# Kernel optimization log

Measured on AMD Instinct MI355X. Metric: run time of the kernel, lower is better.

The kernel has to match this reference:

```python
import jax, jax.numpy as jnp
import numpy as np

B = 16384
D = 1024
NG = 64
H = 2  # num_heads = len(conv_kernel_sizes)


def setup_inputs() -> dict:
    key = jax.random.key(0)
    ks = jax.random.split(key, 12)
    s = 0.02
    return {
        "x": jax.random.normal(ks[0], (B, D), jnp.float32),
        "group_labels": jax.random.randint(ks[1], (B,), 0, NG, dtype=jnp.int32),
        "num_groups": NG,
        "conv_w2": jax.random.normal(ks[2], (2,), jnp.float32) * s,
        "conv_b2": jax.random.normal(ks[3], (), jnp.float32) * s,
        "conv_w4": jax.random.normal(ks[4], (4,), jnp.float32) * s,
        "conv_b4": jax.random.normal(ks[5], (), jnp.float32) * s,
        "intra_in_w": jax.random.normal(ks[6], (3 * D, D), jnp.float32) * s,
        "intra_in_b": jnp.zeros((3 * D,), jnp.float32),
        "intra_out_w": jax.random.normal(ks[7], (D, D), jnp.float32) * s,
        "intra_out_b": jnp.zeros((D,), jnp.float32),
        "inter_in_w": jax.random.normal(ks[8], (3 * D, D), jnp.float32) * s,
        "inter_in_b": jnp.zeros((3 * D,), jnp.float32),
        "inter_out_w": jax.random.normal(ks[9], (D, D), jnp.float32) * s,
        "inter_out_b": jnp.zeros((D,), jnp.float32),
        "lin_w": jax.random.normal(ks[10], (D, D), jnp.float32) * s,
        "lin_b": jnp.zeros((D,), jnp.float32),
    }


def _seg_conv(x_s, l_s, w, b):
    """Per-group Conv2d(1,1,(k,1),padding=(k//2,0)) along the group-sorted axis,
    with zero padding at group boundaries and output trimmed to group size.
    out[i] = sum_j w[j] * x[i + j - k//2] if same group else 0."""
    n = x_s.shape[0]
    k = w.shape[0]
    pad = k // 2
    xp = jnp.pad(x_s, ((pad, pad), (0, 0)))
    lp = jnp.pad(l_s, (pad, pad), constant_values=-1)
    out = jnp.zeros_like(x_s)
    for j in range(k):  # k <= 4, static
        m = (lp[j:j + n] == l_s)[:, None]
        out = out + w[j] * jnp.where(m, xp[j:j + n], 0.0)
    return out + b


def _mha_self(xs, in_w, in_b, out_w, out_b, h):
    """torch nn.MultiheadAttention self-attention, seq-first xs: [S, N, D]."""
    S, N, Dm = xs.shape
    dh = Dm // h
    qkv = jnp.einsum('snd,ed->sne', xs, in_w) + in_b
    q, k, v = jnp.split(qkv, 3, axis=-1)
    q = q.reshape(S, N, h, dh)
    k = k.reshape(S, N, h, dh)
    v = v.reshape(S, N, h, dh)
    scores = jnp.einsum('qnhd,knhd->nhqk', q, k) / np.float32(np.sqrt(dh))
    a = jax.nn.softmax(scores, axis=-1)
    o = jnp.einsum('nhqk,knhd->qnhd', a, v).reshape(S, N, Dm)
    return jnp.einsum('snd,ed->sne', o, out_w) + out_b


def reference(x, group_labels, num_groups, conv_w2, conv_b2, conv_w4, conv_b4,
              intra_in_w, intra_in_b, intra_out_w, intra_out_b,
              inter_in_w, inter_in_b, inter_out_w, inter_out_b, lin_w, lin_b):
    n, d = x.shape
    labels = group_labels.astype(jnp.int32)
    perm = jnp.argsort(labels)  # stable: preserves original order within groups
    x_s = x[perm]
    l_s = labels[perm]

    # per-group convs -> [2, N, D] token stack (seq-first for MHA)
    t2 = _seg_conv(x_s, l_s, conv_w2, conv_b2)
    t4 = _seg_conv(x_s, l_s, conv_w4, conv_b4)
    tok = jnp.stack([t2, t4], axis=0)

    # intra attention over the 2 conv tokens per position, mean, then Linear
    intra = _mha_self(tok, intra_in_w, intra_in_b, intra_out_w, intra_out_b, H).mean(axis=0)
    lin_out = intra @ lin_w.T + lin_b  # [N, D]

    # inter-group: seq-len-1 attention over FIRST row of each other group ==
    # out_proj(v_proj(first_row)); mean over the other present groups.
    counts = jax.ops.segment_sum(jnp.ones((n,), jnp.int32), labels, num_segments=num_groups)
    present = counts > 0
    first_idx = jax.ops.segment_min(jnp.arange(n), labels, num_segments=num_groups)
    first_rows = x[jnp.where(present, first_idx, 0)]  # [NG, D]
    Wv = inter_in_w[2 * d:]
    bv = inter_in_b[2 * d:]
    f = (first_rows @ Wv.T + bv) @ inter_out_w.T + inter_out_b  # [NG, D]
    f = jnp.where(present[:, None], f, 0.0)
    n_present = jnp.sum(present.astype(jnp.int32))
    denom = jnp.maximum(n_present - 1, 1).astype(x.dtype)
    inter_mean = (jnp.sum(f, axis=0)[None, :] - f) / denom
    inter_mean = inter_mean * (n_present > 1).astype(x.dtype)

    out_s = lin_out + inter_mean[l_s]
    return jnp.zeros_like(x).at[perm].set(out_s)
```

## Files before the change

kernel.cpp:

```cpp
#include <hip/hip_runtime.h>
#include <hip/hip_bf16.h>

#define B_N 16384
#define D_DIM 1024
#define NGRP 64
#define NCHUNK 64
#define CHUNK 256

typedef __attribute__((ext_vector_type(8))) short short8;
typedef __attribute__((ext_vector_type(8))) unsigned short ushort8;
typedef __attribute__((ext_vector_type(4))) unsigned short ushort4v;
typedef __attribute__((ext_vector_type(4))) float floatx4;

__device__ __forceinline__ float bf2f(unsigned short h) {
    union { unsigned u; float f; } c; c.u = ((unsigned)h) << 16; return c.f;
}
__device__ __forceinline__ unsigned short f2bf(float f) {
    union { float f; unsigned u; } c; c.f = f;
    unsigned r = c.u + 0x7FFFu + ((c.u >> 16) & 1u);
    return (unsigned short)(r >> 16);
}

__device__ __forceinline__ void gload_lds16(const void* g, void* l) {
    __builtin_amdgcn_global_load_lds(
        (const __attribute__((address_space(1))) unsigned int*)g,
        (__attribute__((address_space(3))) unsigned int*)l, 16, 0, 0);
}

__global__ __launch_bounds__(256) void k_hist(const int* __restrict__ labels,
                                              int* __restrict__ hist) {
    __shared__ int lh[NGRP];
    int t = threadIdx.x, c = blockIdx.x;
    if (t < NGRP) lh[t] = 0;
    __syncthreads();
    int lab = labels[c * CHUNK + t];
    atomicAdd(&lh[lab], 1);
    __syncthreads();
    if (t < NGRP) hist[c * NGRP + t] = lh[t];
}

__global__ void k_scan(int* __restrict__ hist, int* __restrict__ gstart,
                       int* __restrict__ counts, float* __restrict__ scal) {
    __shared__ int cnt[NGRP];
    __shared__ int st[NGRP + 1];
    int g = threadIdx.x;
    int run = 0;
    for (int c = 0; c < NCHUNK; c++) {
        int v = hist[c * NGRP + g];
        hist[c * NGRP + g] = run;
        run += v;
    }
    cnt[g] = run;
    counts[g] = run;
    __syncthreads();
    if (g == 0) {
        int s = 0, np = 0;
        for (int i = 0; i < NGRP; i++) { st[i] = s; s += cnt[i]; np += (cnt[i] > 0); }
        st[NGRP] = s;
        scal[0] = (np > 1) ? 1.0f / (float)(np - 1) : 0.0f;
    }
    __syncthreads();
    gstart[g] = st[g];
    if (g == 0) gstart[NGRP] = st[NGRP];
    for (int c = 0; c < NCHUNK; c++) hist[c * NGRP + g] += st[g];
}

__global__ __launch_bounds__(256) void k_scatter(const int* __restrict__ labels,
                                                 const int* __restrict__ hist,
                                                 int* __restrict__ perm,
                                                 int* __restrict__ ls) {
    __shared__ int lab[CHUNK];
    int c = blockIdx.x, t = threadIdx.x;
    int i = c * CHUNK + t;
    int L = labels[i];
    lab[t] = L;
    __syncthreads();
    int rank = 0;
    for (int j = 0; j < t; j++) rank += (lab[j] == L);
    int pos = hist[c * NGRP + L] + rank;
    perm[pos] = i;
    ls[pos] = L;
}

__global__ __launch_bounds__(256) void k_conv(const float* __restrict__ x,
                                              const int* __restrict__ perm,
                                              const int* __restrict__ ls,
                                              const float* __restrict__ w2, const float* __restrict__ b2,
                                              const float* __restrict__ w4, const float* __restrict__ b4,
                                              unsigned short* __restrict__ tok) {
    const int i = blockIdx.x;
    const int li = ls[i];
    const int p0 = perm[i];
    const int pm1 = (i >= 1 && ls[i - 1] == li) ? perm[i - 1] : -1;
    const int pm2 = (i >= 2 && ls[i - 2] == li) ? perm[i - 2] : -1;
    const int pp1 = (i + 1 < B_N && ls[i + 1] == li) ? perm[i + 1] : -1;
    const int c = threadIdx.x * 4;
    floatx4 z = (floatx4)0.0f;
    floatx4 x0 = *(const floatx4*)(x + (size_t)p0 * D_DIM + c);
    floatx4 xm1 = (pm1 >= 0) ? *(const floatx4*)(x + (size_t)pm1 * D_DIM + c) : z;
    floatx4 xm2 = (pm2 >= 0) ? *(const floatx4*)(x + (size_t)pm2 * D_DIM + c) : z;
    floatx4 xp1 = (pp1 >= 0) ? *(const floatx4*)(x + (size_t)pp1 * D_DIM + c) : z;
    const float w20 = w2[0], w21 = w2[1], cb2 = b2[0];
    const float w40 = w4[0], w41 = w4[1], w42 = w4[2], w43 = w4[3], cb4 = b4[0];
    ushort4v o2, o4;
#pragma unroll
    for (int j = 0; j < 4; j++) {
        float t2 = w20 * xm1[j] + w21 * x0[j] + cb2;
        float t4 = w40 * xm2[j] + w41 * xm1[j] + w42 * x0[j] + w43 * xp1[j] + cb4;
        o2[j] = f2bf(t2);
        o4[j] = f2bf(t4);
    }
    *(ushort4v*)(tok + (size_t)(2 * i) * D_DIM + c) = o2;
    *(ushort4v*)(tok + (size_t)(2 * i + 1) * D_DIM + c) = o4;
}

__global__ __launch_bounds__(256) void k_prep(const float* __restrict__ intra_in_w,
                                              const float* __restrict__ lin_w,
                                              const float* __restrict__ intra_out_w,
                                              unsigned short* __restrict__ Wqk,
                                              unsigned short* __restrict__ linwb,
                                              unsigned short* __restrict__ WoT,
                                              unsigned short* __restrict__ WvT) {
    __shared__ float tile[32][33];
    const int bx = blockIdx.x;
    if (bx < 3072) {
        int i = bx * 256 + threadIdx.x;
        const float* src;
        unsigned short* dst;
        int j;
        if (i < 524288) { src = intra_in_w; dst = Wqk; j = i; }
        else { src = lin_w; dst = linwb; j = i - 524288; }
        floatx4 v = *(const floatx4*)(src + (size_t)j * 4);
        ushort4v o;
#pragma unroll
        for (int q = 0; q < 4; q++) o[q] = f2bf(v[q]);
        *(ushort4v*)(dst + (size_t)j * 4) = o;
    } else {
        int tb = bx - 3072;
        const float* src;
        unsigned short* dst;
        if (tb < 1024) { src = intra_out_w; dst = WoT; }
        else { src = intra_in_w + (size_t)2048 * D_DIM; dst = WvT; tb -= 1024; }
        const int bX = (tb & 31) * 32, bY = (tb >> 5) * 32;
        const int tx = threadIdx.x & 31, ty = threadIdx.x >> 5;
        for (int r = ty; r < 32; r += 8)
            tile[r][tx] = src[(size_t)(bY + r) * D_DIM + bX + tx];
        __syncthreads();
        for (int r = ty; r < 32; r += 8)
            dst[(size_t)(bX + r) * D_DIM + bY + tx] = f2bf(tile[tx][r]);
    }
}

__global__ __launch_bounds__(256) void k_ob2(const float* __restrict__ ow,
                                             const float* __restrict__ ob,
                                             const float* __restrict__ bv,
                                             float* __restrict__ ob2) {
    int e = blockIdx.x * 256 + threadIdx.x;
    const floatx4* wr4 = (const floatx4*)(ow + (size_t)e * D_DIM);
    const floatx4* bv4 = (const floatx4*)bv;
    float s = ob[e];
    for (int k4 = 0; k4 < D_DIM / 4; k4++) {
        floatx4 a = wr4[k4], b = bv4[k4];
        s += a[0] * b[0] + a[1] * b[1] + a[2] * b[2] + a[3] * b[3];
    }
    ob2[e] = s;
}

__global__ __launch_bounds__(256) void k_u(const float* __restrict__ x,
                                           const int* __restrict__ perm,
                                           const int* __restrict__ gstart,
                                           const int* __restrict__ counts,
                                           const float* __restrict__ Wfull,
                                           const float* __restrict__ bfull,
                                           float* __restrict__ u,
                                           const float* __restrict__ lin_w,
                                           const float* __restrict__ lin_b,
                                           const float* __restrict__ ob2,
                                           float* __restrict__ biasc) {
    const int g = blockIdx.y;
    const int n = blockIdx.x * 256 + threadIdx.x;
    __shared__ __align__(16) float xr[D_DIM];
    const bool isb = (g == NGRP);
    int row = 0;
    if (!isb) {
        const int cnt = counts[g];
        row = (cnt > 0) ? perm[gstart[g]] : 0;
    }
    for (int k = threadIdx.x; k < D_DIM; k += 256)
        xr[k] = isb ? ob2[k] : x[(size_t)row * D_DIM + k];
    __syncthreads();
    const float* wrow = isb ? (lin_w + (size_t)n * D_DIM)
                            : (Wfull + (size_t)(2 * D_DIM + n) * D_DIM);
    const floatx4* wr4 = (const floatx4*)wrow;
    const floatx4* xr4 = (const floatx4*)xr;
    float s = isb ? lin_b[n] : bfull[2 * D_DIM + n];
    for (int k4 = 0; k4 < D_DIM / 4; k4++) {
        floatx4 a = xr4[k4], b = wr4[k4];
        s += a[0] * b[0] + a[1] * b[1] + a[2] * b[2] + a[3] * b[3];
    }
    if (isb) biasc[n] = s;
    else u[g * D_DIM + n] = s;
}

__global__ __launch_bounds__(256) void k_f(const float* __restrict__ u,
                                           const int* __restrict__ counts,
                                           const float* __restrict__ W,
                                           const float* __restrict__ b,
                                           float* __restrict__ f) {
    const int g = blockIdx.y;
    const int n = blockIdx.x * 256 + threadIdx.x;
    __shared__ __align__(16) float ur[D_DIM];
    const int cnt = counts[g];
    for (int k = threadIdx.x; k < D_DIM; k += 256) ur[k] = u[g * D_DIM + k];
    __syncthreads();
    const floatx4* wr4 = (const floatx4*)(W + (size_t)n * D_DIM);
    const floatx4* ur4 = (const floatx4*)ur;
    float s = b[n];
    for (int k4 = 0; k4 < D_DIM / 4; k4++) {
        floatx4 a = ur4[k4], w = wr4[k4];
        s += a[0] * w[0] + a[1] * w[1] + a[2] * w[2] + a[3] * w[3];
    }
    f[g * D_DIM + n] = (cnt > 0) ? s : 0.0f;
}

__global__ __launch_bounds__(256) void k_imean(const float* __restrict__ f,
                                               const float* __restrict__ scal,
                                               float* __restrict__ im) {
    int c = blockIdx.x * 256 + threadIdx.x;
    float s = 0.0f;
    for (int g = 0; g < NGRP; g++) s += f[g * D_DIM + c];
    float fl = scal[0];
    for (int g = 0; g < NGRP; g++) im[g * D_DIM + c] = (s - f[g * D_DIM + c]) * fl;
}

template <int MODE>
__global__ __launch_bounds__(256)
void gemm_bt(const unsigned short* __restrict__ A,
             const unsigned short* __restrict__ W,
             int M, int N, int K, int lda, int ldw,
             const float* __restrict__ bias,
             unsigned short* __restrict__ outb, int ldc,
             float* __restrict__ outf,
             const int* __restrict__ perm,
             const int* __restrict__ ls,
             const float* __restrict__ imean) {
    __shared__ __align__(16) unsigned short sA[128 * 64];
    __shared__ __align__(16) unsigned short sB[128 * 64];
    const int t = threadIdx.x;
    const int lane = t & 63, wv = t >> 6;
    int bx = blockIdx.x, by = blockIdx.y;
    const int nX = gridDim.x, nY = gridDim.y;
    if ((nY & 7) == 0) {
        const int bid = by * nX + bx;
        const int xcd = bid & 7, j = bid >> 3;
        const int stripe = nY >> 3;
        by = xcd * stripe + j / nX;
        bx = j % nX;
    }
    const int m0 = by * 128, n0 = bx * 128;
    const int wm = (wv & 1) * 64, wn = (wv >> 1) * 64;
    const int l15 = lane & 15, quad = lane >> 4;
    const int sw = l15 & 7;

    floatx4 acc[4][4];
#pragma unroll
    for (int i = 0; i < 4; i++)
#pragma unroll
        for (int j = 0; j < 4; j++) acc[i][j] = (floatx4)0.0f;

    for (int k0 = 0; k0 < K; k0 += 64) {
#pragma unroll
        for (int r = 0; r < 4; r++) {
            const int chunk = r * 256 + wv * 64;
            const int idx = chunk + lane;
            const int row = idx >> 3;
            const int kb = (idx & 7) ^ (row & 7);
            gload_lds16(A + (size_t)(m0 + row) * lda + k0 + kb * 8, &sA[chunk * 8]);
            gload_lds16(W + (size_t)(n0 + row) * ldw + k0 + kb * 8, &sB[chunk * 8]);
        }
        __syncthreads();
#pragma unroll
        for (int kk = 0; kk < 64; kk += 32) {
            const int kc = kk >> 3;
            short8 av[4], bv[4];
#pragma unroll
            for (int mt = 0; mt < 4; mt++)
                av[mt] = *(const short8*)&sA[(wm + mt * 16 + l15) * 64 +
                                             (((kc + quad) ^ sw) << 3)];
#pragma unroll
            for (int nt = 0; nt < 4; nt++)
                bv[nt] = *(const short8*)&sB[(wn + nt * 16 + l15) * 64 +
                                             (((kc + quad) ^ sw) << 3)];
#pragma unroll
            for (int mt = 0; mt < 4; mt++)
#pragma unroll
                for (int nt = 0; nt < 4; nt++)
                    acc[mt][nt] = __builtin_amdgcn_mfma_f32_16x16x32_bf16(
                        av[mt], bv[nt], acc[mt][nt], 0, 0, 0);
        }
        __syncthreads();
    }

    if (MODE == 1) {
#pragma unroll
        for (int nt = 0; nt < 4; nt++) {
            const int gc = n0 + wn + nt * 16 + l15;
#pragma unroll
            for (int mt = 0; mt < 4; mt++) {
                const int gr = m0 + wm + mt * 16 + quad * 4;
#pragma unroll
                for (int r = 0; r < 4; r++)
                    outb[(size_t)(gr + r) * ldc + gc] = f2bf(acc[mt][nt][r]);
            }
        }
    } else {
        float bb[4];
        int gc4[4];
#pragma unroll
        for (int nt = 0; nt < 4; nt++) {
            gc4[nt] = n0 + wn + nt * 16 + l15;
            bb[nt] = bias[gc4[nt]];
        }
#pragma unroll
        for (int mt = 0; mt < 4; mt++) {
#pragma unroll
            for (int r = 0; r < 4; r++) {
                const int i = m0 + wm + mt * 16 + quad * 4 + r;
                const int orow = perm[i];
                const int lg = ls[i];
#pragma unroll
                for (int nt = 0; nt < 4; nt++)
                    outf[(size_t)orow * N + gc4[nt]] =
                        acc[mt][nt][r] + bb[nt] + imean[lg * D_DIM + gc4[nt]];
            }
        }
    }
}

__global__ __launch_bounds__(256) void k_qkscore(const unsigned short* __restrict__ A,
                                                 const unsigned short* __restrict__ Wq,
                                                 const unsigned short* __restrict__ Wk,
                                                 const float* __restrict__ bq,
                                                 const float* __restrict__ bk,
                                                 floatx4* __restrict__ sp) {
    __shared__ __align__(16) unsigned short sA[128 * 64];
    __shared__ __align__(16) unsigned short sBq[64 * 64];
    __shared__ __align__(16) unsigned short sBk[64 * 64];
    const int t = threadIdx.x;
    const int lane = t & 63, wv = t >> 6;
    int bx = blockIdx.x, by = blockIdx.y;
    {
        const int nX = gridDim.x, nY = gridDim.y;
        const int bid = by * nX + bx;
        const int xcd = bid & 7, j = bid >> 3;
        const int stripe = nY >> 3;
        by = xcd * stripe + j / nX;
        bx = j % nX;
    }
    const int m0 = by * 128, n0 = bx * 64;
    const int wm = (wv & 1) * 64, wn = (wv >> 1) * 32;
    const int l15 = lane & 15, quad = lane >> 4;
    const int sw = l15 & 7;

    floatx4 qa[4][2], ka[4][2];
#pragma unroll
    for (int i = 0; i < 4; i++)
#pragma unroll
        for (int j = 0; j < 2; j++) { qa[i][j] = (floatx4)0.0f; ka[i][j] = (floatx4)0.0f; }

    for (int k0 = 0; k0 < D_DIM; k0 += 64) {
#pragma unroll
        for (int r = 0; r < 4; r++) {
            const int chunk = r * 256 + wv * 64;
            const int idx = chunk + lane;
            const int row = idx >> 3;
            const int kb = (idx & 7) ^ (row & 7);
            gload_lds16(A + (size_t)(m0 + row) * D_DIM + k0 + kb * 8, &sA[chunk * 8]);
        }
#pragma unroll
        for (int r = 0; r < 2; r++) {
            const int chunk = r * 256 + wv * 64;
            const int idx = chunk + lane;
            const int row = idx >> 3;
            const int kb = (idx & 7) ^ (row & 7);
            gload_lds16(Wq + (size_t)(n0 + row) * D_DIM + k0 + kb * 8, &sBq[chunk * 8]);
            gload_lds16(Wk + (size_t)(n0 + row) * D_DIM + k0 + kb * 8, &sBk[chunk * 8]);
        }
        __syncthreads();
#pragma unroll
        for (int kk = 0; kk < 64; kk += 32) {
            const int kc = kk >> 3;
            short8 av[4], bqv[2], bkv[2];
#pragma unroll
            for (int mt = 0; mt < 4; mt++)
                av[mt] = *(const short8*)&sA[(wm + mt * 16 + l15) * 64 +
                                             (((kc + quad) ^ sw) << 3)];
#pragma unroll
            for (int nt = 0; nt < 2; nt++) {
                bqv[nt] = *(const short8*)&sBq[(wn + nt * 16 + l15) * 64 +
                                               (((kc + quad) ^ sw) << 3)];
                bkv[nt] = *(const short8*)&sBk[(wn + nt * 16 + l15) * 64 +
                                               (((kc + quad) ^ sw) << 3)];
            }
#pragma unroll
            for (int mt = 0; mt < 4; mt++)
#pragma unroll
                for (int nt = 0; nt < 2; nt++) {
                    qa[mt][nt] = __builtin_amdgcn_mfma_f32_16x16x32_bf16(
                        av[mt], bqv[nt], qa[mt][nt], 0, 0, 0);
                    ka[mt][nt] = __builtin_amdgcn_mfma_f32_16x16x32_bf16(
                        av[mt], bkv[nt], ka[mt][nt], 0, 0, 0);
                }
        }
        __syncthreads();
    }

    float bqv2[2], bkv2[2];
#pragma unroll
    for (int nt = 0; nt < 2; nt++) {
        const int col = n0 + wn + nt * 16 + l15;
        bqv2[nt] = bq[col];
        bkv2[nt] = bk[col];
    }
#pragma unroll
    for (int mt = 0; mt < 4; mt++) {
#pragma unroll
        for (int p = 0; p < 2; p++) {
            float s22 = 0, s24 = 0, s42 = 0, s44 = 0;
#pragma unroll
            for (int nt = 0; nt < 2; nt++) {
                float q0 = qa[mt][nt][2 * p] + bqv2[nt];
                float q1 = qa[mt][nt][2 * p + 1] + bqv2[nt];
                float k0v = ka[mt][nt][2 * p] + bkv2[nt];
                float k1v = ka[mt][nt][2 * p + 1] + bkv2[nt];
                s22 += q0 * k0v; s24 += q0 * k1v; s42 += q1 * k0v; s44 += q1 * k1v;
            }
#pragma unroll
            for (int d = 1; d < 16; d <<= 1) {
                s22 += __shfl_xor(s22, d, 64);
                s24 += __shfl_xor(s24, d, 64);
                s42 += __shfl_xor(s42, d, 64);
                s44 += __shfl_xor(s44, d, 64);
            }
            if (l15 == 0) {
                const int i = (m0 + wm + mt * 16 + quad * 4 + 2 * p) >> 1;
                floatx4 v;
                v[0] = s22; v[1] = s24; v[2] = s42; v[3] = s44;
                sp[(size_t)bx * B_N + i] = v;
            }
        }
    }
}

__global__ __launch_bounds__(256) void k_gam(const floatx4* __restrict__ sp,
                                             floatx4* __restrict__ gam) {
    const int i = blockIdx.x * 256 + threadIdx.x;
    float a[8];
#pragma unroll
    for (int j = 0; j < 8; j++) a[j] = 0.0f;
#pragma unroll
    for (int b = 0; b < 16; b++) {
        floatx4 v = sp[(size_t)b * B_N + i];
        const int h4 = (b >> 3) * 4;
        a[h4 + 0] += v[0]; a[h4 + 1] += v[1]; a[h4 + 2] += v[2]; a[h4 + 3] += v[3];
    }
    const float sc = 0.044194173824159216f;
    floatx4 g;
#pragma unroll
    for (int h = 0; h < 2; h++) {
        float s22 = a[h * 4 + 0] * sc, s24 = a[h * 4 + 1] * sc;
        float s42 = a[h * 4 + 2] * sc, s44 = a[h * 4 + 3] * sc;
        float m0 = fmaxf(s22, s24), e22 = __expf(s22 - m0), e24 = __expf(s24 - m0);
        float w24 = e24 / (e22 + e24), w22 = 1.0f - w24;
        float m1 = fmaxf(s42, s44), e42 = __expf(s42 - m1), e44 = __expf(s44 - m1);
        float w44 = e44 / (e42 + e44), w42 = 1.0f - w44;
        g[h * 2 + 0] = 0.5f * (w22 + w42);
        g[h * 2 + 1] = 0.5f * (w24 + w44);
    }
    gam[i] = g;
}

__global__ __launch_bounds__(256) void k_zprep(unsigned short* __restrict__ tok,
                                               const floatx4* __restrict__ gam) {
    const int idx = blockIdx.x * 256 + threadIdx.x;
    const int i = idx >> 7;
    const int seg = (idx & 127) * 8;
    floatx4 g = gam[i];
    short8 a = *(const short8*)(tok + (size_t)(2 * i) * D_DIM + seg);
    short8 b = *(const short8*)(tok + (size_t)(2 * i + 1) * D_DIM + seg);
    ushort8 z1, z2;
#pragma unroll
    for (int j = 0; j < 8; j++) {
        float af = bf2f((unsigned short)a[j]), bf = bf2f((unsigned short)b[j]);
        z1[j] = f2bf(g[0] * af + g[1] * bf);
        z2[j] = f2bf(g[2] * af + g[3] * bf);
    }
    *(ushort8*)(tok + (size_t)(2 * i) * D_DIM + seg) = z1;
    *(ushort8*)(tok + (size_t)(2 * i + 1) * D_DIM + seg) = z2;
}

extern "C" void kernel_launch(void* const* d_in, const int* in_sizes, int n_in,
                              void* d_out, int out_size, void* d_ws, size_t ws_size,
                              hipStream_t stream) {
    const float* x = (const float*)d_in[0];
    const int* labels = (const int*)d_in[1];
    const float* conv_w2 = (const float*)d_in[3];
    const float* conv_b2 = (const float*)d_in[4];
    const float* conv_w4 = (const float*)d_in[5];
    const float* conv_b4 = (const float*)d_in[6];
    const float* intra_in_w = (const float*)d_in[7];
    const float* intra_in_b = (const float*)d_in[8];
    const float* intra_out_w = (const float*)d_in[9];
    const float* intra_out_b = (const float*)d_in[10];
    const float* inter_in_w = (const float*)d_in[11];
    const float* inter_in_b = (const float*)d_in[12];
    const float* inter_out_w = (const float*)d_in[13];
    const float* inter_out_b = (const float*)d_in[14];
    const float* lin_w = (const float*)d_in[15];
    const float* lin_b = (const float*)d_in[16];
    float* out = (float*)d_out;

    char* p = (char*)d_ws;
    auto alloc = [&](size_t bytes) -> void* {
        void* r = (void*)p;
        p += (bytes + 255) & ~(size_t)255;
        return r;
    };
    int* perm = (int*)alloc(B_N * 4);
    int* lss = (int*)alloc(B_N * 4);
    int* hist = (int*)alloc(NCHUNK * NGRP * 4);
    int* gstart = (int*)alloc((NGRP + 1) * 4);
    int* counts = (int*)alloc(NGRP * 4);
    float* scal = (float*)alloc(4);
    unsigned short* tok = (unsigned short*)alloc((size_t)2 * B_N * D_DIM * 2);
    unsigned short* Wqk = (unsigned short*)alloc((size_t)2 * D_DIM * D_DIM * 2);
    unsigned short* linwb = (unsigned short*)alloc((size_t)D_DIM * D_DIM * 2);
    unsigned short* WoT = (unsigned short*)alloc((size_t)D_DIM * D_DIM * 2);
    unsigned short* WvT = (unsigned short*)alloc((size_t)D_DIM * D_DIM * 2);
    unsigned short* Wc = (unsigned short*)alloc((size_t)D_DIM * D_DIM * 2);
    unsigned short* GG = (unsigned short*)alloc((size_t)D_DIM * 2 * D_DIM * 2);
    floatx4* sp = (floatx4*)alloc((size_t)16 * B_N * 16);
    floatx4* gam = (floatx4*)alloc((size_t)B_N * 16);
    float* u = (float*)alloc((size_t)NGRP * D_DIM * 4);
    float* fbuf = (float*)alloc((size_t)NGRP * D_DIM * 4);
    float* imean = (float*)alloc((size_t)NGRP * D_DIM * 4);
    float* biasc = (float*)alloc(D_DIM * 4);
    float* ob2 = (float*)alloc(D_DIM * 4);

    k_hist<<<NCHUNK, CHUNK, 0, stream>>>(labels, hist);
    k_scan<<<1, NGRP, 0, stream>>>(hist, gstart, counts, scal);
    k_scatter<<<NCHUNK, CHUNK, 0, stream>>>(labels, hist, perm, lss);
    k_prep<<<3072 + 2048, 256, 0, stream>>>(intra_in_w, lin_w, intra_out_w, Wqk, linwb,
                                            WoT, WvT);
    gemm_bt<1><<<dim3(8, 8), 256, 0, stream>>>(linwb, WoT, 1024, 1024, 1024, 1024, 1024,
                                               nullptr, Wc, 1024, nullptr, nullptr,
                                               nullptr, nullptr);
    gemm_bt<1><<<dim3(8, 8), 256, 0, stream>>>(Wc, WvT, 1024, 1024, 512, 1024, 1024,
                                               nullptr, GG, 2048, nullptr, nullptr,
                                               nullptr, nullptr);
    gemm_bt<1><<<dim3(8, 8), 256, 0, stream>>>(Wc + 512, WvT + 512, 1024, 1024, 512, 1024,
                                               1024, nullptr, GG + 1024, 2048, nullptr,
                                               nullptr, nullptr, nullptr);
    k_ob2<<<4, 256, 0, stream>>>(intra_out_w, intra_out_b, intra_in_b + 2 * D_DIM, ob2);
    k_u<<<dim3(4, NGRP + 1), 256, 0, stream>>>(x, perm, gstart, counts, inter_in_w,
                                               inter_in_b, u, lin_w, lin_b, ob2, biasc);
    k_f<<<dim3(4, NGRP), 256, 0, stream>>>(u, counts, inter_out_w, inter_out_b, fbuf);
    k_imean<<<4, 256, 0, stream>>>(fbuf, scal, imean);
    k_conv<<<B_N, 256, 0, stream>>>(x, perm, lss, conv_w2, conv_b2, conv_w4, conv_b4, tok);
    k_qkscore<<<dim3(16, 256), 256, 0, stream>>>(tok, Wqk, Wqk + (size_t)D_DIM * D_DIM,
                                                 intra_in_b, intra_in_b + D_DIM, sp);
    k_gam<<<B_N / 256, 256, 0, stream>>>(sp, gam);
    k_zprep<<<B_N / 2, 256, 0, stream>>>(tok, gam);
    gemm_bt<2><<<dim3(8, 128), 256, 0, stream>>>(tok, GG, B_N, 1024, 2048, 2048, 2048,
                                                 biasc, nullptr, 0, out, perm, lss, imean);
}
```

Baseline: 625.1 us.

## Merge small launches and reuse neighbor rows in conv kernel

The conv kernel now handles four consecutive sorted rows per block, loading a sliding window of seven input rows instead of four loads per output row, which cuts redundant gathers of x. The ob2 bias reduction moves into the k_prep launch as extra blocks. The two half-K GEMMs that build GG become one launch through a new mode that offsets A and W for the upper column tiles. The gamma softmax is fused into the z-prep kernel. Together these remove several kernel launches and the gam buffer round trip, at the cost of more registers in conv and some redundant per-block work in the fused kernels.

```diff
diff --git a/kernel.cpp b/kernel.cpp
--- a/kernel.cpp
+++ b/kernel.cpp
@@ -88,39 +88,52 @@
                                               const float* __restrict__ w2, const float* __restrict__ b2,
                                               const float* __restrict__ w4, const float* __restrict__ b4,
                                               unsigned short* __restrict__ tok) {
-    const int i = blockIdx.x;
-    const int li = ls[i];
-    const int p0 = perm[i];
-    const int pm1 = (i >= 1 && ls[i - 1] == li) ? perm[i - 1] : -1;
-    const int pm2 = (i >= 2 && ls[i - 2] == li) ? perm[i - 2] : -1;
-    const int pp1 = (i + 1 < B_N && ls[i + 1] == li) ? perm[i + 1] : -1;
+    const int i0 = blockIdx.x * 4;
     const int c = threadIdx.x * 4;
-    floatx4 z = (floatx4)0.0f;
-    floatx4 x0 = *(const floatx4*)(x + (size_t)p0 * D_DIM + c);
-    floatx4 xm1 = (pm1 >= 0) ? *(const floatx4*)(x + (size_t)pm1 * D_DIM + c) : z;
-    floatx4 xm2 = (pm2 >= 0) ? *(const floatx4*)(x + (size_t)pm2 * D_DIM + c) : z;
-    floatx4 xp1 = (pp1 >= 0) ? *(const floatx4*)(x + (size_t)pp1 * D_DIM + c) : z;
+    int lab[7];
+    floatx4 xr[7];
+    const floatx4 z = (floatx4)0.0f;
+#pragma unroll
+    for (int j = 0; j < 7; j++) {
+        const int idx = i0 + j - 2;
+        const bool v = (idx >= 0 && idx < B_N);
+        lab[j] = v ? ls[idx] : -1;
+        const int pr = v ? perm[idx] : 0;
+        xr[j] = v ? *(const floatx4*)(x + (size_t)pr * D_DIM + c) : z;
+    }
     const float w20 = w2[0], w21 = w2[1], cb2 = b2[0];
     const float w40 = w4[0], w41 = w4[1], w42 = w4[2], w43 = w4[3], cb4 = b4[0];
-    ushort4v o2, o4;
-#pragma unroll
-    for (int j = 0; j < 4; j++) {
-        float t2 = w20 * xm1[j] + w21 * x0[j] + cb2;
-        float t4 = w40 * xm2[j] + w41 * xm1[j] + w42 * x0[j] + w43 * xp1[j] + cb4;
-        o2[j] = f2bf(t2);
-        o4[j] = f2bf(t4);
-    }
-    *(ushort4v*)(tok + (size_t)(2 * i) * D_DIM + c) = o2;
-    *(ushort4v*)(tok + (size_t)(2 * i + 1) * D_DIM + c) = o4;
+#pragma unroll
+    for (int k = 0; k < 4; k++) {
+        const int li = lab[k + 2];
+        floatx4 m2 = (lab[k] == li) ? xr[k] : z;
+        floatx4 m1 = (lab[k + 1] == li) ? xr[k + 1] : z;
+        floatx4 x0 = xr[k + 2];
+        floatx4 p1 = (lab[k + 3] == li) ? xr[k + 3] : z;
+        ushort4v o2, o4;
+#pragma unroll
+        for (int j = 0; j < 4; j++) {
+            float t2 = w20 * m1[j] + w21 * x0[j] + cb2;
+            float t4 = w40 * m2[j] + w41 * m1[j] + w42 * x0[j] + w43 * p1[j] + cb4;
+            o2[j] = f2bf(t2);
+            o4[j] = f2bf(t4);
+        }
+        const int i = i0 + k;
+        *(ushort4v*)(tok + (size_t)(2 * i) * D_DIM + c) = o2;
+        *(ushort4v*)(tok + (size_t)(2 * i + 1) * D_DIM + c) = o4;
+    }
 }
 
 __global__ __launch_bounds__(256) void k_prep(const float* __restrict__ intra_in_w,
                                               const float* __restrict__ lin_w,
                                               const float* __restrict__ intra_out_w,
+                                              const float* __restrict__ intra_out_b,
                                               unsigned short* __restrict__ Wqk,
                                               unsigned short* __restrict__ linwb,
                                               unsigned short* __restrict__ WoT,
-                                              unsigned short* __restrict__ WvT) {
+                                              unsigned short* __restrict__ WvT,
+                                              const float* __restrict__ bv,
+                                              float* __restrict__ ob2) {
     __shared__ float tile[32][33];
     const int bx = blockIdx.x;
     if (bx < 3072) {
@@ -135,7 +148,7 @@
 #pragma unroll
         for (int q = 0; q < 4; q++) o[q] = f2bf(v[q]);
         *(ushort4v*)(dst + (size_t)j * 4) = o;
-    } else {
+    } else if (bx < 5120) {
         int tb = bx - 3072;
         const float* src;
         unsigned short* dst;
@@ -148,22 +161,17 @@
         __syncthreads();
         for (int r = ty; r < 32; r += 8)
             dst[(size_t)(bX + r) * D_DIM + bY + tx] = f2bf(tile[tx][r]);
-    }
-}
-
-__global__ __launch_bounds__(256) void k_ob2(const float* __restrict__ ow,
-                                             const float* __restrict__ ob,
-                                             const float* __restrict__ bv,
-                                             float* __restrict__ ob2) {
-    int e = blockIdx.x * 256 + threadIdx.x;
-    const floatx4* wr4 = (const floatx4*)(ow + (size_t)e * D_DIM);
-    const floatx4* bv4 = (const floatx4*)bv;
-    float s = ob[e];
-    for (int k4 = 0; k4 < D_DIM / 4; k4++) {
-        floatx4 a = wr4[k4], b = bv4[k4];
-        s += a[0] * b[0] + a[1] * b[1] + a[2] * b[2] + a[3] * b[3];
-    }
-    ob2[e] = s;
+    } else {
+        const int e = (bx - 5120) * 256 + threadIdx.x;
+        const floatx4* wr4 = (const floatx4*)(intra_out_w + (size_t)e * D_DIM);
+        const floatx4* bv4 = (const floatx4*)bv;
+        float s = intra_out_b[e];
+        for (int k4 = 0; k4 < D_DIM / 4; k4++) {
+            floatx4 a = wr4[k4], b = bv4[k4];
+            s += a[0] * b[0] + a[1] * b[1] + a[2] * b[2] + a[3] * b[3];
+        }
+        ob2[e] = s;
+    }
 }
 
 __global__ __launch_bounds__(256) void k_u(const float* __restrict__ x,
@@ -258,6 +266,12 @@
         bx = j % nX;
     }
     const int m0 = by * 128, n0 = bx * 128;
+    const unsigned short* Ap = A;
+    const unsigned short* Wp = W + (size_t)n0 * ldw;
+    if (MODE == 3 && n0 >= 1024) {
+        Ap = A + 512;
+        Wp = W + (size_t)(n0 - 1024) * ldw + 512;
+    }
     const int wm = (wv & 1) * 64, wn = (wv >> 1) * 64;
     const int l15 = lane & 15, quad = lane >> 4;
     const int sw = l15 & 7;
@@ -275,8 +289,8 @@
             const int idx = chunk + lane;
             const int row = idx >> 3;
             const int kb = (idx & 7) ^ (row & 7);
-            gload_lds16(A + (size_t)(m0 + row) * lda + k0 + kb * 8, &sA[chunk * 8]);
-            gload_lds16(W + (size_t)(n0 + row) * ldw + k0 + kb * 8, &sB[chunk * 8]);
+            gload_lds16(Ap + (size_t)(m0 + row) * lda + k0 + kb * 8, &sA[chunk * 8]);
+            gload_lds16(Wp + (size_t)row * ldw + k0 + kb * 8, &sB[chunk * 8]);
         }
         __syncthreads();
 #pragma unroll
@@ -301,7 +315,7 @@
         __syncthreads();
     }
 
-    if (MODE == 1) {
+    if (MODE != 2) {
 #pragma unroll
         for (int nt = 0; nt < 4; nt++) {
             const int gc = n0 + wn + nt * 16 + l15;
@@ -452,46 +466,47 @@
     }
 }
 
-__global__ __launch_bounds__(256) void k_gam(const floatx4* __restrict__ sp,
-                                             floatx4* __restrict__ gam) {
-    const int i = blockIdx.x * 256 + threadIdx.x;
-    float a[8];
-#pragma unroll
-    for (int j = 0; j < 8; j++) a[j] = 0.0f;
-#pragma unroll
-    for (int b = 0; b < 16; b++) {
-        floatx4 v = sp[(size_t)b * B_N + i];
-        const int h4 = (b >> 3) * 4;
-        a[h4 + 0] += v[0]; a[h4 + 1] += v[1]; a[h4 + 2] += v[2]; a[h4 + 3] += v[3];
-    }
-    const float sc = 0.044194173824159216f;
-    floatx4 g;
-#pragma unroll
-    for (int h = 0; h < 2; h++) {
-        float s22 = a[h * 4 + 0] * sc, s24 = a[h * 4 + 1] * sc;
-        float s42 = a[h * 4 + 2] * sc, s44 = a[h * 4 + 3] * sc;
-        float m0 = fmaxf(s22, s24), e22 = __expf(s22 - m0), e24 = __expf(s24 - m0);
-        float w24 = e24 / (e22 + e24), w22 = 1.0f - w24;
-        float m1 = fmaxf(s42, s44), e42 = __expf(s42 - m1), e44 = __expf(s44 - m1);
-        float w44 = e44 / (e42 + e44), w42 = 1.0f - w44;
-        g[h * 2 + 0] = 0.5f * (w22 + w42);
-        g[h * 2 + 1] = 0.5f * (w24 + w44);
-    }
-    gam[i] = g;
-}
-
-__global__ __launch_bounds__(256) void k_zprep(unsigned short* __restrict__ tok,
-                                               const floatx4* __restrict__ gam) {
-    const int idx = blockIdx.x * 256 + threadIdx.x;
-    const int i = idx >> 7;
-    const int seg = (idx & 127) * 8;
-    floatx4 g = gam[i];
+__global__ __launch_bounds__(256) void k_zgam(unsigned short* __restrict__ tok,
+                                              const floatx4* __restrict__ sp) {
+    __shared__ floatx4 lg[2];
+    const int b = blockIdx.x;
+    const int t = threadIdx.x;
+    if (t < 2) {
+        const int i = b * 2 + t;
+        float a[8];
+#pragma unroll
+        for (int j = 0; j < 8; j++) a[j] = 0.0f;
+#pragma unroll
+        for (int q = 0; q < 16; q++) {
+            floatx4 v = sp[(size_t)q * B_N + i];
+            const int h4 = (q >> 3) * 4;
+            a[h4 + 0] += v[0]; a[h4 + 1] += v[1]; a[h4 + 2] += v[2]; a[h4 + 3] += v[3];
+        }
+        const float sc = 0.044194173824159216f;
+        floatx4 g;
+#pragma unroll
+        for (int h = 0; h < 2; h++) {
+            float s22 = a[h * 4 + 0] * sc, s24 = a[h * 4 + 1] * sc;
+            float s42 = a[h * 4 + 2] * sc, s44 = a[h * 4 + 3] * sc;
+            float m0 = fmaxf(s22, s24), e22 = __expf(s22 - m0), e24 = __expf(s24 - m0);
+            float w24 = e24 / (e22 + e24), w22 = 1.0f - w24;
+            float m1 = fmaxf(s42, s44), e42 = __expf(s42 - m1), e44 = __expf(s44 - m1);
+            float w44 = e44 / (e42 + e44), w42 = 1.0f - w44;
+            g[h * 2 + 0] = 0.5f * (w22 + w42);
+            g[h * 2 + 1] = 0.5f * (w24 + w44);
+        }
+        lg[t] = g;
+    }
+    __syncthreads();
+    const int i = b * 2 + (t >> 7);
+    const int seg = (t & 127) * 8;
+    floatx4 g = lg[t >> 7];
     short8 a = *(const short8*)(tok + (size_t)(2 * i) * D_DIM + seg);
-    short8 b = *(const short8*)(tok + (size_t)(2 * i + 1) * D_DIM + seg);
+    short8 bb = *(const short8*)(tok + (size_t)(2 * i + 1) * D_DIM + seg);
     ushort8 z1, z2;
 #pragma unroll
     for (int j = 0; j < 8; j++) {
-        float af = bf2f((unsigned short)a[j]), bf = bf2f((unsigned short)b[j]);
+        float af = bf2f((unsigned short)a[j]), bf = bf2f((unsigned short)bb[j]);
         z1[j] = f2bf(g[0] * af + g[1] * bf);
         z2[j] = f2bf(g[2] * af + g[3] * bf);
     }
@@ -540,7 +555,6 @@
     unsigned short* Wc = (unsigned short*)alloc((size_t)D_DIM * D_DIM * 2);
     unsigned short* GG = (unsigned short*)alloc((size_t)D_DIM * 2 * D_DIM * 2);
     floatx4* sp = (floatx4*)alloc((size_t)16 * B_N * 16);
-    floatx4* gam = (floatx4*)alloc((size_t)B_N * 16);
     float* u = (float*)alloc((size_t)NGRP * D_DIM * 4);
     float* fbuf = (float*)alloc((size_t)NGRP * D_DIM * 4);
     float* imean = (float*)alloc((size_t)NGRP * D_DIM * 4);
@@ -550,27 +564,23 @@
     k_hist<<<NCHUNK, CHUNK, 0, stream>>>(labels, hist);
     k_scan<<<1, NGRP, 0, stream>>>(hist, gstart, counts, scal);
     k_scatter<<<NCHUNK, CHUNK, 0, stream>>>(labels, hist, perm, lss);
-    k_prep<<<3072 + 2048, 256, 0, stream>>>(intra_in_w, lin_w, intra_out_w, Wqk, linwb,
-                                            WoT, WvT);
+    k_prep<<<5124, 256, 0, stream>>>(intra_in_w, lin_w, intra_out_w, intra_out_b, Wqk,
+                                     linwb, WoT, WvT, intra_in_b + 2 * D_DIM, ob2);
     gemm_bt<1><<<dim3(8, 8), 256, 0, stream>>>(linwb, WoT, 1024, 1024, 1024, 1024, 1024,
                                                nullptr, Wc, 1024, nullptr, nullptr,
                                                nullptr, nullptr);
-    gemm_bt<1><<<dim3(8, 8), 256, 0, stream>>>(Wc, WvT, 1024, 1024, 512, 1024, 1024,
-                                               nullptr, GG, 2048, nullptr, nullptr,
-                                               nullptr, nullptr);
-    gemm_bt<1><<<dim3(8, 8), 256, 0, stream>>>(Wc + 512, WvT + 512, 1024, 1024, 512, 1024,
-                                               1024, nullptr, GG + 1024, 2048, nullptr,
-                                               nullptr, nullptr, nullptr);
-    k_ob2<<<4, 256, 0, stream>>>(intra_out_w, intra_out_b, intra_in_b + 2 * D_DIM, ob2);
+    gemm_bt<3><<<dim3(16, 8), 256, 0, stream>>>(Wc, WvT, 1024, 2048, 512, 1024, 1024,
+                                                nullptr, GG, 2048, nullptr, nullptr,
+                                                nullptr, nullptr);
     k_u<<<dim3(4, NGRP + 1), 256, 0, stream>>>(x, perm, gstart, counts, inter_in_w,
                                                inter_in_b, u, lin_w, lin_b, ob2, biasc);
     k_f<<<dim3(4, NGRP), 256, 0, stream>>>(u, counts, inter_out_w, inter_out_b, fbuf);
     k_imean<<<4, 256, 0, stream>>>(fbuf, scal, imean);
-    k_conv<<<B_N, 256, 0, stream>>>(x, perm, lss, conv_w2, conv_b2, conv_w4, conv_b4, tok);
+    k_conv<<<B_N / 4, 256, 0, stream>>>(x, perm, lss, conv_w2, conv_b2, conv_w4, conv_b4,
+                                        tok);
     k_qkscore<<<dim3(16, 256), 256, 0, stream>>>(tok, Wqk, Wqk + (size_t)D_DIM * D_DIM,
                                                  intra_in_b, intra_in_b + D_DIM, sp);
-    k_gam<<<B_N / 256, 256, 0, stream>>>(sp, gam);
-    k_zprep<<<B_N / 2, 256, 0, stream>>>(tok, gam);
+    k_zgam<<<B_N / 2, 256, 0, stream>>>(tok, sp);
     gemm_bt<2><<<dim3(8, 128), 256, 0, stream>>>(tok, GG, B_N, 1024, 2048, 2048, 2048,
                                                  biasc, nullptr, 0, out, perm, lss, imean);
 }
```

Result: faster. 599.6 us (-4.1%).
